# Optimization experiments

Measured on AMD Instinct MI355X. Metric: run time of the kernel, lower is better.

Reference implementation:

```python
import jax, jax.numpy as jnp
import numpy as np

B, N, F_IN, F_OUT = 16, 1024, 128, 128

def setup_inputs() -> dict:
    key = jax.random.key(0)
    k1, k2, k3 = jax.random.split(key, 3)
    X = jax.random.normal(k1, (B, N, F_IN), dtype=jnp.float32)
    A = jax.random.uniform(k2, (B, N, N), dtype=jnp.float32)
    W = jax.random.normal(k3, (F_IN, F_OUT), dtype=jnp.float32)
    return {"X": X, "A": A, "W": W}

def reference(X, A, W):
    # A_hat = A + I  (batched add of identity)
    n = A.shape[-1]
    A_hat = A + jnp.eye(n, dtype=A.dtype)  # [B,N,N]
    # D_hat^{-1/2} applied as elementwise row/col scaling (torch builds diag
    # matrices and inverts; mathematically identical for diagonal D).
    deg = jnp.sum(A_hat, axis=-1)               # [B,N]
    d_inv_sqrt = 1.0 / jnp.sqrt(deg)            # [B,N]
    A_norm = A_hat * d_inv_sqrt[:, :, None] * d_inv_sqrt[:, None, :]  # [B,N,N]
    out = jnp.einsum('bnm,bmf->bnf', A_norm, X)  # aggregation bmm
    out = jnp.einsum('bnf,fg->bng', out, W)      # weight matmul
    return out
```

## Files before the change

kernel.cpp:

```cpp
#include <hip/hip_runtime.h>

#define NN 1024
#define FF 128

typedef __attribute__((ext_vector_type(8))) short bf16x8;
typedef __attribute__((ext_vector_type(4))) float f32x4;

__device__ __forceinline__ unsigned short f2bf(float x) {
  unsigned u = __float_as_uint(x);
  u += 0x7fff + ((u >> 16) & 1);
  return (unsigned short)(u >> 16);
}
__device__ __forceinline__ float bf2f(unsigned short b) {
  return __uint_as_float(((unsigned)b) << 16);
}
__device__ __forceinline__ bf16x8 cvt8(float4 a, float4 b) {
  bf16x8 r;
  r[0] = (short)f2bf(a.x); r[1] = (short)f2bf(a.y);
  r[2] = (short)f2bf(a.z); r[3] = (short)f2bf(a.w);
  r[4] = (short)f2bf(b.x); r[5] = (short)f2bf(b.y);
  r[6] = (short)f2bf(b.z); r[7] = (short)f2bf(b.w);
  return r;
}

__device__ __forceinline__ void gl_lds16(const void* g, void* l) {
  __builtin_amdgcn_global_load_lds(
      (const __attribute__((address_space(1))) unsigned*)g,
      (__attribute__((address_space(3))) unsigned*)l, 16, 0, 0);
}

__global__ __launch_bounds__(256) void k_deg(const float* __restrict__ A,
                                             const float* __restrict__ W,
                                             float* __restrict__ d,
                                             unsigned short* __restrict__ Wt) {
  if (blockIdx.x >= 4096) {
    int id = (blockIdx.x - 4096) * 256 + threadIdx.x;
    int g = id >> 7, f = id & 127;
    Wt[g * 128 + f] = f2bf(W[f * 128 + g]);
    return;
  }
  int row  = blockIdx.x * 4 + (threadIdx.x >> 6);
  int lane = threadIdx.x & 63;
  const float4* Ar = (const float4*)(A + (size_t)row * NN);
  float s = 0.f;
#pragma unroll
  for (int i = 0; i < 4; ++i) {
    float4 v = Ar[lane + i * 64];
    s += (v.x + v.y) + (v.z + v.w);
  }
#pragma unroll
  for (int off = 32; off > 0; off >>= 1) s += __shfl_down(s, off, 64);
  if (lane == 0) d[row] = rsqrtf(s + 1.0f);
}

__global__ __launch_bounds__(256) void k_xw(const float* __restrict__ X,
                                            const unsigned short* __restrict__ Wt,
                                            const float* __restrict__ d,
                                            unsigned short* __restrict__ Yt) {
  __shared__ __align__(16) unsigned short Xs[64 * 128];
  __shared__ __align__(16) unsigned short Ws[128 * 128];
  __shared__ float dl[64];
  int t  = threadIdx.x;
  int b  = blockIdx.x >> 4;
  int m0 = (blockIdx.x & 15) * 64;

#pragma unroll
  for (int j = 0; j < 4; ++j) {
    int id = t + j * 256;
    int r = id >> 4, p = id & 15, c = p ^ (r & 15);
    const float* gp = X + ((size_t)(b * NN + m0 + r) * FF + c * 8);
    float4 v0 = *(const float4*)gp;
    float4 v1 = *(const float4*)(gp + 4);
    *(bf16x8*)&Xs[r * 128 + p * 8] = cvt8(v0, v1);
  }
#pragma unroll
  for (int j = 0; j < 8; ++j) {
    int id = t + j * 256;
    int g = id >> 4, p = id & 15, c = p ^ (g & 15);
    uint4 v = *(const uint4*)(Wt + g * 128 + c * 8);
    *(uint4*)&Ws[g * 128 + p * 8] = v;
  }
  if (t < 64) dl[t] = d[b * NN + m0 + t];
  __syncthreads();

  int wave = t >> 6, lane = t & 63, quad = lane >> 4, l16 = lane & 15;
  f32x4 acc[8];
#pragma unroll
  for (int ct = 0; ct < 8; ++ct) acc[ct] = (f32x4){0.f, 0.f, 0.f, 0.f};

#pragma unroll
  for (int ks = 0; ks < 4; ++ks) {
    int q = ks * 4 + quad;
    bf16x8 a = *(const bf16x8*)&Xs[(wave * 16 + l16) * 128 + (q ^ l16) * 8];
#pragma unroll
    for (int ct = 0; ct < 8; ++ct) {
      bf16x8 w = *(const bf16x8*)&Ws[(ct * 16 + l16) * 128 + (q ^ l16) * 8];
      acc[ct] = __builtin_amdgcn_mfma_f32_16x16x32_bf16(a, w, acc[ct], 0, 0, 0);
    }
  }

  int mb = wave * 16 + quad * 4;
  float4 d4 = *(const float4*)&dl[mb];
#pragma unroll
  for (int ct = 0; ct < 8; ++ct) {
    int g = ct * 16 + l16;
    ushort4 p;
    p.x = f2bf(d4.x * acc[ct][0]);
    p.y = f2bf(d4.y * acc[ct][1]);
    p.z = f2bf(d4.z * acc[ct][2]);
    p.w = f2bf(d4.w * acc[ct][3]);
    *(ushort4*)(Yt + (size_t)(b * 128 + g) * NN + m0 + mb) = p;
  }
}

__global__ __launch_bounds__(256) void k_agg(const float* __restrict__ A,
                                             const unsigned short* __restrict__ Yt,
                                             const float* __restrict__ d,
                                             float* __restrict__ out) {
  __shared__ __align__(16) float          Asf[32 * 128];
  __shared__ __align__(16) unsigned short Ys[128 * 128];
  int t   = threadIdx.x;
  int bid = blockIdx.x;
  int xcd = bid & 7;
  int j   = bid >> 3;
  int b   = xcd + 8 * (j >> 5);
  int n0  = (j & 31) * 32;
  int wave = t >> 6, lane = t & 63, quad = lane >> 4, l16 = lane & 15;
  int wr = wave >> 1, wc = wave & 1;
  int rl = lane >> 4, pl = lane & 15;
  int rh = lane >> 5, cc = lane & 31;

  const float*          Ab = A  + (size_t)(b * NN + n0) * NN;
  const unsigned short* Yb = Yt + (size_t)b * 128 * NN;

  auto issue = [&](int k0) {
#pragma unroll
    for (int jj = 0; jj < 4; ++jj) {
      int r0 = wave * 8 + jj * 2;
      int r  = r0 + rh;
      int c  = cc ^ (2 * (r & 15));
      gl_lds16(Ab + ((size_t)r * NN + k0 + c * 4), &Asf[r0 * 128]);
    }
#pragma unroll
    for (int jj = 0; jj < 8; ++jj) {
      int r0 = wave * 32 + jj * 4;
      int r  = r0 + rl;
      int c  = pl ^ (r & 15);
      gl_lds16(Yb + ((size_t)r * NN + k0 + c * 8), &Ys[r0 * 128]);
    }
  };

  f32x4 acc[4];
#pragma unroll
  for (int ct = 0; ct < 4; ++ct) acc[ct] = (f32x4){0.f, 0.f, 0.f, 0.f};

  int swA = 2 * l16;
  issue(0);
  for (int s = 0; s < 8; ++s) {
    __syncthreads();
#pragma unroll
    for (int ks = 0; ks < 4; ++ks) {
      int cq = ks * 4 + quad;
      int pa = (2 * cq) ^ swA;
      float4 a0 = *(const float4*)&Asf[(wr * 16 + l16) * 128 + pa * 4];
      float4 a1 = *(const float4*)&Asf[(wr * 16 + l16) * 128 + pa * 4 + 4];
      bf16x8 a = cvt8(a0, a1);
#pragma unroll
      for (int ct = 0; ct < 4; ++ct) {
        bf16x8 y = *(const bf16x8*)&Ys[(wc * 64 + ct * 16 + l16) * 128 + ((cq ^ l16)) * 8];
        acc[ct] = __builtin_amdgcn_mfma_f32_16x16x32_bf16(a, y, acc[ct], 0, 0, 0);
      }
    }
    __syncthreads();
    if (s < 7) issue((s + 1) * 128);
  }

  int nb = n0 + wr * 16 + quad * 4;
  float4 d4 = *(const float4*)(d + b * NN + nb);
#pragma unroll
  for (int ct = 0; ct < 4; ++ct) {
    int g = wc * 64 + ct * 16 + l16;
    ushort4 yv = *(const ushort4*)(Yt + (size_t)(b * 128 + g) * NN + nb);
    float* op = out + ((size_t)(b * NN + nb) * FF + g);
    op[0 * FF] = d4.x * (acc[ct][0] + bf2f(yv.x));
    op[1 * FF] = d4.y * (acc[ct][1] + bf2f(yv.y));
    op[2 * FF] = d4.z * (acc[ct][2] + bf2f(yv.z));
    op[3 * FF] = d4.w * (acc[ct][3] + bf2f(yv.w));
  }
}

extern "C" void kernel_launch(void* const* d_in, const int* in_sizes, int n_in,
                              void* d_out, int out_size, void* d_ws, size_t ws_size,
                              hipStream_t stream) {
  const float* X = (const float*)d_in[0];
  const float* A = (const float*)d_in[1];
  const float* W = (const float*)d_in[2];
  float* out = (float*)d_out;

  char* ws = (char*)d_ws;
  float*          dinv = (float*)ws;
  unsigned short* Wt   = (unsigned short*)(ws + 65536);
  unsigned short* Yt   = (unsigned short*)(ws + 98304);

  k_deg<<<dim3(4096 + 64), dim3(256), 0, stream>>>(A, W, dinv, Wt);
  k_xw <<<dim3(256),       dim3(256), 0, stream>>>(X, Wt, dinv, Yt);
  k_agg<<<dim3(512),       dim3(256), 0, stream>>>(A, Yt, dinv, out);
}
```

Before: 119.6 us.

## Merge degree and XW kernels, apply column scaling in aggregation

The degree-reduction and X·W GEMM run as independent blocks of one launch, and the W transpose/convert moves into each GEMM block's LDS. That removes one kernel launch and the dependency of XW on the degree vector. Column scaling by d^{-1/2} moves into the aggregation kernel, which multiplies the A tile by d values held in LDS before the bf16 conversion. The cost is extra multiplies and LDS reads in the inner loop, plus every XW block redundantly transposing W.

```diff
diff --git a/kernel.cpp b/kernel.cpp
--- a/kernel.cpp
+++ b/kernel.cpp
@@ -29,38 +29,31 @@
       (__attribute__((address_space(3))) unsigned*)l, 16, 0, 0);
 }
 
-__global__ __launch_bounds__(256) void k_deg(const float* __restrict__ A,
+__global__ __launch_bounds__(256) void k_pre(const float* __restrict__ A,
+                                             const float* __restrict__ X,
                                              const float* __restrict__ W,
                                              float* __restrict__ d,
-                                             unsigned short* __restrict__ Wt) {
-  if (blockIdx.x >= 4096) {
-    int id = (blockIdx.x - 4096) * 256 + threadIdx.x;
-    int g = id >> 7, f = id & 127;
-    Wt[g * 128 + f] = f2bf(W[f * 128 + g]);
+                                             unsigned short* __restrict__ Yt) {
+  __shared__ __align__(16) unsigned short Xs[64 * 128];
+  __shared__ __align__(16) unsigned short Wl[128 * 128];
+  int t = threadIdx.x;
+  int wave = t >> 6, lane = t & 63;
+
+  if (blockIdx.x >= 256) {
+    int row = (blockIdx.x - 256) * 4 + wave;
+    const float4* Ar = (const float4*)(A + (size_t)row * NN);
+    float s = 0.f;
+#pragma unroll
+    for (int i = 0; i < 4; ++i) {
+      float4 v = Ar[lane + i * 64];
+      s += (v.x + v.y) + (v.z + v.w);
+    }
+#pragma unroll
+    for (int off = 32; off > 0; off >>= 1) s += __shfl_down(s, off, 64);
+    if (lane == 0) d[row] = rsqrtf(s + 1.0f);
     return;
   }
-  int row  = blockIdx.x * 4 + (threadIdx.x >> 6);
-  int lane = threadIdx.x & 63;
-  const float4* Ar = (const float4*)(A + (size_t)row * NN);
-  float s = 0.f;
-#pragma unroll
-  for (int i = 0; i < 4; ++i) {
-    float4 v = Ar[lane + i * 64];
-    s += (v.x + v.y) + (v.z + v.w);
-  }
-#pragma unroll
-  for (int off = 32; off > 0; off >>= 1) s += __shfl_down(s, off, 64);
-  if (lane == 0) d[row] = rsqrtf(s + 1.0f);
-}
-
-__global__ __launch_bounds__(256) void k_xw(const float* __restrict__ X,
-                                            const unsigned short* __restrict__ Wt,
-                                            const float* __restrict__ d,
-                                            unsigned short* __restrict__ Yt) {
-  __shared__ __align__(16) unsigned short Xs[64 * 128];
-  __shared__ __align__(16) unsigned short Ws[128 * 128];
-  __shared__ float dl[64];
-  int t  = threadIdx.x;
+
   int b  = blockIdx.x >> 4;
   int m0 = (blockIdx.x & 15) * 64;
 
@@ -74,16 +67,21 @@
     *(bf16x8*)&Xs[r * 128 + p * 8] = cvt8(v0, v1);
   }
 #pragma unroll
-  for (int j = 0; j < 8; ++j) {
-    int id = t + j * 256;
-    int g = id >> 4, p = id & 15, c = p ^ (g & 15);
-    uint4 v = *(const uint4*)(Wt + g * 128 + c * 8);
-    *(uint4*)&Ws[g * 128 + p * 8] = v;
-  }
-  if (t < 64) dl[t] = d[b * NN + m0 + t];
+  for (int j = 0; j < 16; ++j) {
+    int id4 = t + j * 256;
+    int f = id4 >> 5, g4 = (id4 & 31) * 4;
+    float4 v = *(const float4*)(W + f * 128 + g4);
+    unsigned short pv[4];
+    pv[0] = f2bf(v.x); pv[1] = f2bf(v.y); pv[2] = f2bf(v.z); pv[3] = f2bf(v.w);
+#pragma unroll
+    for (int i = 0; i < 4; ++i) {
+      int g = g4 + i;
+      Wl[g * 128 + (((f >> 3) ^ (g & 15)) << 3) + (f & 7)] = pv[i];
+    }
+  }
   __syncthreads();
 
-  int wave = t >> 6, lane = t & 63, quad = lane >> 4, l16 = lane & 15;
+  int quad = lane >> 4, l16 = lane & 15;
   f32x4 acc[8];
 #pragma unroll
   for (int ct = 0; ct < 8; ++ct) acc[ct] = (f32x4){0.f, 0.f, 0.f, 0.f};
@@ -94,21 +92,20 @@
     bf16x8 a = *(const bf16x8*)&Xs[(wave * 16 + l16) * 128 + (q ^ l16) * 8];
 #pragma unroll
     for (int ct = 0; ct < 8; ++ct) {
-      bf16x8 w = *(const bf16x8*)&Ws[(ct * 16 + l16) * 128 + (q ^ l16) * 8];
+      bf16x8 w = *(const bf16x8*)&Wl[(ct * 16 + l16) * 128 + (q ^ l16) * 8];
       acc[ct] = __builtin_amdgcn_mfma_f32_16x16x32_bf16(a, w, acc[ct], 0, 0, 0);
     }
   }
 
   int mb = wave * 16 + quad * 4;
-  float4 d4 = *(const float4*)&dl[mb];
 #pragma unroll
   for (int ct = 0; ct < 8; ++ct) {
     int g = ct * 16 + l16;
     ushort4 p;
-    p.x = f2bf(d4.x * acc[ct][0]);
-    p.y = f2bf(d4.y * acc[ct][1]);
-    p.z = f2bf(d4.z * acc[ct][2]);
-    p.w = f2bf(d4.w * acc[ct][3]);
+    p.x = f2bf(acc[ct][0]);
+    p.y = f2bf(acc[ct][1]);
+    p.z = f2bf(acc[ct][2]);
+    p.w = f2bf(acc[ct][3]);
     *(ushort4*)(Yt + (size_t)(b * 128 + g) * NN + m0 + mb) = p;
   }
 }
@@ -119,6 +116,7 @@
                                              float* __restrict__ out) {
   __shared__ __align__(16) float          Asf[32 * 128];
   __shared__ __align__(16) unsigned short Ys[128 * 128];
+  __shared__ __align__(16) float          dl[NN];
   int t   = threadIdx.x;
   int bid = blockIdx.x;
   int xcd = bid & 7;
@@ -133,6 +131,8 @@
   const float*          Ab = A  + (size_t)(b * NN + n0) * NN;
   const unsigned short* Yb = Yt + (size_t)b * 128 * NN;
 
+  *(float4*)&dl[t * 4] = *(const float4*)(d + (size_t)b * NN + t * 4);
+
   auto issue = [&](int k0) {
 #pragma unroll
     for (int jj = 0; jj < 4; ++jj) {
@@ -154,6 +154,7 @@
 #pragma unroll
   for (int ct = 0; ct < 4; ++ct) acc[ct] = (f32x4){0.f, 0.f, 0.f, 0.f};
 
+  const float4* dl4 = (const float4*)dl;
   int swA = 2 * l16;
   issue(0);
   for (int s = 0; s < 8; ++s) {
@@ -164,10 +165,14 @@
       int pa = (2 * cq) ^ swA;
       float4 a0 = *(const float4*)&Asf[(wr * 16 + l16) * 128 + pa * 4];
       float4 a1 = *(const float4*)&Asf[(wr * 16 + l16) * 128 + pa * 4 + 4];
+      float4 dm0 = dl4[s * 32 + cq * 2];
+      float4 dm1 = dl4[s * 32 + cq * 2 + 1];
+      a0.x *= dm0.x; a0.y *= dm0.y; a0.z *= dm0.z; a0.w *= dm0.w;
+      a1.x *= dm1.x; a1.y *= dm1.y; a1.z *= dm1.z; a1.w *= dm1.w;
       bf16x8 a = cvt8(a0, a1);
 #pragma unroll
       for (int ct = 0; ct < 4; ++ct) {
-        bf16x8 y = *(const bf16x8*)&Ys[(wc * 64 + ct * 16 + l16) * 128 + ((cq ^ l16)) * 8];
+        bf16x8 y = *(const bf16x8*)&Ys[(wc * 64 + ct * 16 + l16) * 128 + (cq ^ l16) * 8];
         acc[ct] = __builtin_amdgcn_mfma_f32_16x16x32_bf16(a, y, acc[ct], 0, 0, 0);
       }
     }
@@ -176,16 +181,16 @@
   }
 
   int nb = n0 + wr * 16 + quad * 4;
-  float4 d4 = *(const float4*)(d + b * NN + nb);
+  float4 d4 = dl4[nb >> 2];
 #pragma unroll
   for (int ct = 0; ct < 4; ++ct) {
     int g = wc * 64 + ct * 16 + l16;
     ushort4 yv = *(const ushort4*)(Yt + (size_t)(b * 128 + g) * NN + nb);
     float* op = out + ((size_t)(b * NN + nb) * FF + g);
-    op[0 * FF] = d4.x * (acc[ct][0] + bf2f(yv.x));
-    op[1 * FF] = d4.y * (acc[ct][1] + bf2f(yv.y));
-    op[2 * FF] = d4.z * (acc[ct][2] + bf2f(yv.z));
-    op[3 * FF] = d4.w * (acc[ct][3] + bf2f(yv.w));
+    op[0 * FF] = d4.x * (acc[ct][0] + d4.x * bf2f(yv.x));
+    op[1 * FF] = d4.y * (acc[ct][1] + d4.y * bf2f(yv.y));
+    op[2 * FF] = d4.z * (acc[ct][2] + d4.z * bf2f(yv.z));
+    op[3 * FF] = d4.w * (acc[ct][3] + d4.w * bf2f(yv.w));
   }
 }
 
@@ -199,10 +204,8 @@
 
   char* ws = (char*)d_ws;
   float*          dinv = (float*)ws;
-  unsigned short* Wt   = (unsigned short*)(ws + 65536);
-  unsigned short* Yt   = (unsigned short*)(ws + 98304);
-
-  k_deg<<<dim3(4096 + 64), dim3(256), 0, stream>>>(A, W, dinv, Wt);
-  k_xw <<<dim3(256),       dim3(256), 0, stream>>>(X, Wt, dinv, Yt);
-  k_agg<<<dim3(512),       dim3(256), 0, stream>>>(A, Yt, dinv, out);
-}
+  unsigned short* Yt   = (unsigned short*)(ws + 65536);
+
+  k_pre<<<dim3(256 + 4096), dim3(256), 0, stream>>>(A, X, W, dinv, Yt);
+  k_agg<<<dim3(512),        dim3(256), 0, stream>>>(A, Yt, dinv, out);
+}
```

Result: slower. 122.9 us (+2.8%).
